# Performance work log

Hardware: AMD Instinct MI355X
Metric: run time of the kernel (lower is better)

## Reference

```python
import jax, jax.numpy as jnp
import numpy as np

NB = 8            # num_blocks
D = 128           # embed_dim
D_INNER = 256     # expand=2
HEADS = 4
P = 64            # headdim
N = 32            # d_state
K = 4             # d_conv
CONV_DIM = D_INNER + 2 * N          # 320 (x, B, C streams)
D_IN_PROJ = 2 * D_INNER + 2 * N + HEADS  # 580 (z, xBC, dt)


def setup_inputs():
    key = jax.random.key(0)
    ks = iter(jax.random.split(key, 16))
    f = lambda shape, s=0.02: (jax.random.normal(next(ks), shape, jnp.float32) * s)
    B, L = 2, 4096
    return {
        'x': jax.random.normal(next(ks), (B, L, D), jnp.float32),
        'residual': jnp.zeros((B, L, D), jnp.float32),
        'ln1_w': jnp.ones((NB, D)), 'ln1_b': jnp.zeros((NB, D)),
        'ln2_w': jnp.ones((NB, D)), 'ln2_b': jnp.zeros((NB, D)),
        'fc1_w': f((NB, 4 * D, D)), 'fc1_b': jnp.zeros((NB, 4 * D)),
        'fc2_w': f((NB, D, 2 * D)), 'fc2_b': jnp.zeros((NB, D)),
        'in_proj_w': f((NB, D_IN_PROJ, D)),
        'conv_w': f((NB, CONV_DIM, K), 0.1), 'conv_b': jnp.zeros((NB, CONV_DIM)),
        'dt_bias': f((NB, HEADS), 0.1),
        'A_log': jnp.tile(jnp.log(jnp.arange(1, HEADS + 1, dtype=jnp.float32)), (NB, 1)),
        'Dp': jnp.ones((NB, HEADS)),
        'rms_w': jnp.ones((NB, D_INNER)),
        'out_proj_w': f((NB, D, D_INNER)),
        'h': 64, 'w': 64,
    }


def layernorm(x, w, b):
    mu = jnp.mean(x, -1, keepdims=True)
    var = jnp.mean((x - mu) ** 2, -1, keepdims=True)
    return (x - mu) * jax.lax.rsqrt(var + 1e-5) * w + b


def mamba2(x, in_proj_w, conv_w, conv_b, dt_bias, A_log, Dp, rms_w, out_proj_w):
    Bb, L, _ = x.shape
    zxbcdt = jnp.einsum('bld,ed->ble', x, in_proj_w)          # [B,L,580]
    z = zxbcdt[..., :D_INNER]
    xBC = zxbcdt[..., D_INNER:D_INNER + CONV_DIM]
    dt = jax.nn.softplus(zxbcdt[..., -HEADS:] + dt_bias)      # [B,L,H]
    # causal depthwise conv1d + silu
    xc = jnp.moveaxis(xBC, 1, 2)                              # [B,C,L]
    xc = jax.lax.conv_general_dilated(xc, conv_w[:, None, :], (1,), [(K - 1, 0)],
                                      feature_group_count=CONV_DIM)
    xBC = jax.nn.silu(jnp.moveaxis(xc, 1, 2) + conv_b)
    xs = xBC[..., :D_INNER].reshape(Bb, L, HEADS, P)          # [B,L,H,P]
    Bm = xBC[..., D_INNER:D_INNER + N]                        # [B,L,N]
    Cm = xBC[..., D_INNER + N:]                               # [B,L,N]
    dA = jnp.exp(dt * (-jnp.exp(A_log)))                      # [B,L,H]

    def step(hst, inp):
        dA_t, dt_t, B_t, C_t, x_t = inp
        hst = hst * dA_t[:, :, None, None] + (dt_t[:, :, None, None] * x_t[..., None]) * B_t[:, None, None, :]
        return hst, jnp.einsum('bhpn,bn->bhp', hst, C_t)

    tfirst = lambda a: jnp.moveaxis(a, 1, 0)
    h0 = jnp.zeros((Bb, HEADS, P, N), x.dtype)
    _, ys = jax.lax.scan(step, h0, (tfirst(dA), tfirst(dt), tfirst(Bm), tfirst(Cm), tfirst(xs)))
    y = jnp.moveaxis(ys, 0, 1) + Dp[None, None, :, None] * xs # [B,L,H,P]
    y = y.reshape(Bb, L, D_INNER) * jax.nn.silu(z)            # gated
    y = y * jax.lax.rsqrt(jnp.mean(y * y, -1, keepdims=True) + 1e-5) * rms_w
    return jnp.einsum('be,de->bd'.replace('b', 'bl'), y, out_proj_w)


def mlp(x, fc1_w, fc1_b, fc2_w, fc2_b):
    x12 = jnp.einsum('bld,ed->ble', x, fc1_w) + fc1_b
    x1, x2 = jnp.split(x12, 2, axis=-1)
    return jnp.einsum('ble,de->bld', jax.nn.silu(x1) * x2, fc2_w) + fc2_b


def reference(x, residual, ln1_w, ln1_b, ln2_w, ln2_b, fc1_w, fc1_b, fc2_w, fc2_b,
              in_proj_w, conv_w, conv_b, dt_bias, A_log, Dp, rms_w, out_proj_w, h, w):
    for i in range(NB):
        residual = x
        x1 = layernorm(residual, ln1_w[i], ln1_b[i])
        x_m = residual + mamba2(x1, in_proj_w[i], conv_w[i], conv_b[i], dt_bias[i],
                                A_log[i], Dp[i], rms_w[i], out_proj_w[i])
        residual = x_m
        x2 = layernorm(residual, ln2_w[i], ln2_b[i])
        x = residual + mlp(x2, fc1_w[i], fc1_b[i], fc2_w[i], fc2_b[i])
    return (x, residual)
```

## Files before the change

### kernel.cpp

```cpp
#include <hip/hip_runtime.h>
#include <hip/hip_bf16.h>
#include <cstddef>

#define NBLK 8
#define DD   128
#define DI   256
#define NH   4
#define PP   64
#define NNs  32
#define CONVD 320
#define EE   580
#define BB   2
#define LLEN 4096
#define ML   (BB*LLEN)
#define SEGS 256
#define TT   16
#define GPAD 264

typedef unsigned short u16;
typedef short bf16x8 __attribute__((ext_vector_type(8)));
typedef float f32x4 __attribute__((ext_vector_type(4)));

__device__ __forceinline__ float siluf(float x){ return x / (1.f + expf(-x)); }
__device__ __forceinline__ float b2f(u16 u){ return __uint_as_float((unsigned)u << 16); }
__device__ __forceinline__ u16 f2b(float f){
    __hip_bfloat16 h = __float2bfloat16(f);
    return *reinterpret_cast<u16*>(&h);
}
__device__ __forceinline__ void ld8f(const u16* p, float* f){
    ushort4 a = *(const ushort4*)p;
    ushort4 b = *(const ushort4*)(p + 4);
    f[0]=b2f(a.x); f[1]=b2f(a.y); f[2]=b2f(a.z); f[3]=b2f(a.w);
    f[4]=b2f(b.x); f[5]=b2f(b.y); f[6]=b2f(b.z); f[7]=b2f(b.w);
}

#define IPW_N (NBLK*EE*DD)
#define OPW_N (NBLK*DD*DI)
#define F1W_N (NBLK*512*DD)
#define F2W_N (NBLK*DD*DI)
#define CVT_TOT (IPW_N+OPW_N+F1W_N+F2W_N)

__global__ __launch_bounds__(256) void cvt_weights(const float* __restrict__ ip,
                                                   const float* __restrict__ op,
                                                   const float* __restrict__ f1,
                                                   const float* __restrict__ f2,
                                                   const float* __restrict__ xin,
                                                   u16* __restrict__ dip,
                                                   u16* __restrict__ dop,
                                                   u16* __restrict__ df1,
                                                   u16* __restrict__ df2,
                                                   float* __restrict__ xout)
{
    int i = blockIdx.x * 256 + threadIdx.x;
    if (i < IPW_N)                          dip[i] = f2b(ip[i]);
    else if (i < IPW_N + OPW_N)             dop[i - IPW_N] = f2b(op[i - IPW_N]);
    else if (i < IPW_N + OPW_N + F1W_N)     df1[i - IPW_N - OPW_N] = f2b(f1[i - IPW_N - OPW_N]);
    else                                    df2[i - IPW_N - OPW_N - F1W_N] = f2b(f2[i - IPW_N - OPW_N - F1W_N]);
    if (i < ML * DD) xout[i] = xin[i];
}

__global__ __launch_bounds__(256) void inproj_ln_gemm(const float* __restrict__ X,
                                                      const float* __restrict__ lnw,
                                                      const float* __restrict__ lnb,
                                                      const u16* __restrict__ W,
                                                      u16* __restrict__ C)
{
    __shared__ __align__(16) u16 Ash[64*128];
    __shared__ __align__(16) u16 Wsh[64*128];
    __shared__ float red[64][8];
    const int tid = threadIdx.x;
    const int wave = tid >> 6, lane = tid & 63;
    const int l15 = lane & 15, quad = lane >> 4;
    const int bm = blockIdx.y * 64;
    const int bn = blockIdx.x * 64;
    const int lrow = tid >> 2, sub = tid & 3;

#pragma unroll
    for (int i = 0; i < 4; i++) {
        int k8 = sub + 4*i;
        uint4 wv = make_uint4(0u,0u,0u,0u);
        if (bn + lrow < EE)
            wv = *(const uint4*)(W + (size_t)(bn + lrow) * DD + k8*8);
        *(uint4*)&Wsh[((size_t)k8*64 + lrow) * 8] = wv;
    }

    const float* xr = X + (size_t)(bm + lrow) * DD + sub*32;
    float4 xv[8];
    float ps = 0.f, pq = 0.f;
#pragma unroll
    for (int i = 0; i < 8; i++) {
        xv[i] = *(const float4*)(xr + i*4);
        ps += xv[i].x + xv[i].y + xv[i].z + xv[i].w;
        pq += xv[i].x*xv[i].x + xv[i].y*xv[i].y + xv[i].z*xv[i].z + xv[i].w*xv[i].w;
    }
    red[lrow][sub] = ps; red[lrow][4+sub] = pq;
    __syncthreads();
    float s = red[lrow][0]+red[lrow][1]+red[lrow][2]+red[lrow][3];
    float q = red[lrow][4]+red[lrow][5]+red[lrow][6]+red[lrow][7];
    float mu = s * (1.f/DD);
    float rstd = rsqrtf(q*(1.f/DD) - mu*mu + 1e-5f);
#pragma unroll
    for (int i = 0; i < 4; i++) {
        float4 a0 = xv[2*i], a1 = xv[2*i+1];
        int c0 = sub*32 + i*8;
        u16 o[8];
        o[0] = f2b((a0.x-mu)*rstd*lnw[c0+0] + lnb[c0+0]);
        o[1] = f2b((a0.y-mu)*rstd*lnw[c0+1] + lnb[c0+1]);
        o[2] = f2b((a0.z-mu)*rstd*lnw[c0+2] + lnb[c0+2]);
        o[3] = f2b((a0.w-mu)*rstd*lnw[c0+3] + lnb[c0+3]);
        o[4] = f2b((a1.x-mu)*rstd*lnw[c0+4] + lnb[c0+4]);
        o[5] = f2b((a1.y-mu)*rstd*lnw[c0+5] + lnb[c0+5]);
        o[6] = f2b((a1.z-mu)*rstd*lnw[c0+6] + lnb[c0+6]);
        o[7] = f2b((a1.w-mu)*rstd*lnw[c0+7] + lnb[c0+7]);
        *(uint4*)&Ash[((size_t)(sub*4+i)*64 + lrow) * 8] = *(uint4*)o;
    }
    __syncthreads();

    f32x4 acc[4];
#pragma unroll
    for (int nt = 0; nt < 4; nt++) acc[nt] = (f32x4){0.f,0.f,0.f,0.f};
#pragma unroll
    for (int kk = 0; kk < 4; kk++) {
        bf16x8 af = *(const bf16x8*)&Ash[(((kk*4 + quad)*64) + wave*16 + l15) * 8];
#pragma unroll
        for (int nt = 0; nt < 4; nt++) {
            bf16x8 bfv = *(const bf16x8*)&Wsh[(((kk*4 + quad)*64) + nt*16 + l15) * 8];
            acc[nt] = __builtin_amdgcn_mfma_f32_16x16x32_bf16(af, bfv, acc[nt], 0, 0, 0);
        }
    }
#pragma unroll
    for (int nt = 0; nt < 4; nt++) {
        int n = bn + nt*16 + l15;
        if (n < EE) {
#pragma unroll
            for (int r = 0; r < 4; r++) {
                int m = bm + wave*16 + quad*4 + r;
                C[(size_t)m * EE + n] = f2b(acc[nt][r]);
            }
        }
    }
}

__global__ __launch_bounds__(256) void scan1(const u16* __restrict__ zx,
                                             const float* __restrict__ cw,
                                             const float* __restrict__ cb,
                                             const float* __restrict__ dt_bias,
                                             const float* __restrict__ A_log,
                                             float* __restrict__ seg,
                                             float* __restrict__ segsum)
{
    __shared__ float Bsh[4][TT*NNs];
    __shared__ float dts[4][TT], das[4][TT];
    int wv = threadIdx.x >> 6;
    int p = threadIdx.x & 63;
    int sg = blockIdx.x % (SEGS/4);
    int bh = blockIdx.x / (SEGS/4);
    int h = bh % NH;
    int b = bh / NH;
    int s = sg*4 + wv;
    int l0 = s * TT;
    int row0 = b * LLEN + l0;

    float xr[TT+3];
    const u16* xcol = zx + (size_t)row0 * EE + 256 + h*64 + p;
#pragma unroll
    for (int r = 0; r < TT+3; r++) {
        int l = l0 - 3 + r;
        xr[r] = (l >= 0) ? b2f(xcol[(ptrdiff_t)(r-3) * EE]) : 0.f;
    }
    float4 wx = *(const float4*)(cw + (size_t)(h*64+p) * 4);
    float cbx = cb[h*64+p];

    if (p < NNs) {
        float br[TT+3];
        const u16* bcol = zx + (size_t)row0 * EE + 512 + p;
#pragma unroll
        for (int r = 0; r < TT+3; r++) {
            int l = l0 - 3 + r;
            br[r] = (l >= 0) ? b2f(bcol[(ptrdiff_t)(r-3) * EE]) : 0.f;
        }
        float4 wb = *(const float4*)(cw + (size_t)(256+p) * 4);
        float cbb = cb[256+p];
#pragma unroll
        for (int t = 0; t < TT; t++)
            Bsh[wv][t*NNs + p] = siluf(cbb + wb.x*br[t] + wb.y*br[t+1] + wb.z*br[t+2] + wb.w*br[t+3]);
    }
    if (p < TT) {
        float v = b2f(zx[(size_t)(row0+p)*EE + (EE-NH) + h]) + dt_bias[h];
        float dt = (v > 20.f) ? v : log1pf(expf(v));
        dts[wv][p] = dt;
        das[wv][p] = expf(-expf(A_log[h]) * dt);
    }
    __syncthreads();

    float hreg[NNs];
#pragma unroll
    for (int n = 0; n < NNs; n++) hreg[n] = 0.f;
    float sdt = 0.f;
#pragma unroll
    for (int t = 0; t < TT; t++) {
        float dA = das[wv][t];
        float dt = dts[wv][t];
        float xv = siluf(cbx + wx.x*xr[t] + wx.y*xr[t+1] + wx.z*xr[t+2] + wx.w*xr[t+3]);
        float dtx = dt * xv;
#pragma unroll
        for (int n4 = 0; n4 < 8; n4++) {
            float4 Bv = *(const float4*)&Bsh[wv][t*NNs + n4*4];
            hreg[n4*4+0] = fmaf(hreg[n4*4+0], dA, dtx * Bv.x);
            hreg[n4*4+1] = fmaf(hreg[n4*4+1], dA, dtx * Bv.y);
            hreg[n4*4+2] = fmaf(hreg[n4*4+2], dA, dtx * Bv.z);
            hreg[n4*4+3] = fmaf(hreg[n4*4+3], dA, dtx * Bv.w);
        }
        sdt += dt;
    }
    int bidg = bh * SEGS + s;
    float* dst = seg + ((size_t)bidg * PP + p) * NNs;
#pragma unroll
    for (int n4 = 0; n4 < 8; n4++)
        *(float4*)(dst + n4*4) = make_float4(hreg[n4*4+0], hreg[n4*4+1], hreg[n4*4+2], hreg[n4*4+3]);
    if (p == 0) segsum[bidg] = sdt;
}

__global__ __launch_bounds__(256) void scan2(float* __restrict__ seg,
                                             const float* __restrict__ segsum,
                                             const float* __restrict__ A_log)
{
    int bh = blockIdx.x >> 3;
    int chunk = blockIdx.x & 7;
    int h = bh % NH;
    int entry = chunk * 256 + threadIdx.x;
    float negA = -expf(A_log[h]);
    float hs = 0.f;
    const float* ss = segsum + bh * SEGS;
    float* base = seg + (size_t)bh * SEGS * (PP * NNs) + entry;
    for (int j0 = 0; j0 < SEGS; j0 += 16) {
        float e[16], a[16];
#pragma unroll
        for (int k = 0; k < 16; k++) {
            a[k] = ss[j0 + k];
            e[k] = base[(size_t)(j0 + k) * (PP * NNs)];
        }
#pragma unroll
        for (int k = 0; k < 16; k++) {
            float Aj = expf(negA * a[k]);
            base[(size_t)(j0 + k) * (PP * NNs)] = hs;
            hs = fmaf(Aj, hs, e[k]);
        }
    }
}

__global__ __launch_bounds__(256) void scan3(const u16* __restrict__ zx,
                                             const float* __restrict__ cw,
                                             const float* __restrict__ cb,
                                             const float* __restrict__ dt_bias,
                                             const float* __restrict__ A_log,
                                             const float* __restrict__ seg,
                                             const float* __restrict__ Dp,
                                             u16* __restrict__ y)
{
    __shared__ float BCsh[4][TT*64];
    __shared__ float dts[4][TT], das[4][TT];
    int wv = threadIdx.x >> 6;
    int p = threadIdx.x & 63;
    int sg = blockIdx.x % (SEGS/4);
    int bh = blockIdx.x / (SEGS/4);
    int h = bh % NH;
    int b = bh / NH;
    int s = sg*4 + wv;
    int l0 = s * TT;
    int row0 = b * LLEN + l0;

    float xr[TT+3];
    const u16* xcol = zx + (size_t)row0 * EE + 256 + h*64 + p;
#pragma unroll
    for (int r = 0; r < TT+3; r++) {
        int l = l0 - 3 + r;
        xr[r] = (l >= 0) ? b2f(xcol[(ptrdiff_t)(r-3) * EE]) : 0.f;
    }
    float4 wx = *(const float4*)(cw + (size_t)(h*64+p) * 4);
    float cbx = cb[h*64+p];

    {
        float br[TT+3];
        const u16* bcol = zx + (size_t)row0 * EE + 512 + p;
#pragma unroll
        for (int r = 0; r < TT+3; r++) {
            int l = l0 - 3 + r;
            br[r] = (l >= 0) ? b2f(bcol[(ptrdiff_t)(r-3) * EE]) : 0.f;
        }
        float4 wb = *(const float4*)(cw + (size_t)(256+p) * 4);
        float cbb = cb[256+p];
#pragma unroll
        for (int t = 0; t < TT; t++)
            BCsh[wv][t*64 + p] = siluf(cbb + wb.x*br[t] + wb.y*br[t+1] + wb.z*br[t+2] + wb.w*br[t+3]);
    }
    if (p < TT) {
        float v = b2f(zx[(size_t)(row0+p)*EE + (EE-NH) + h]) + dt_bias[h];
        float dt = (v > 20.f) ? v : log1pf(expf(v));
        dts[wv][p] = dt;
        das[wv][p] = expf(-expf(A_log[h]) * dt);
    }

    float hreg[NNs];
    int bidg = bh * SEGS + s;
    const float* src = seg + ((size_t)bidg * PP + p) * NNs;
#pragma unroll
    for (int n4 = 0; n4 < 8; n4++) {
        float4 v = *(const float4*)(src + n4*4);
        hreg[n4*4+0] = v.x; hreg[n4*4+1] = v.y; hreg[n4*4+2] = v.z; hreg[n4*4+3] = v.w;
    }
    float dp = Dp[h];
    __syncthreads();

#pragma unroll
    for (int t = 0; t < TT; t++) {
        float dA = das[wv][t];
        float dt = dts[wv][t];
        float xv = siluf(cbx + wx.x*xr[t] + wx.y*xr[t+1] + wx.z*xr[t+2] + wx.w*xr[t+3]);
        float dtx = dt * xv;
        float acc = 0.f;
#pragma unroll
        for (int n4 = 0; n4 < 8; n4++) {
            float4 Bv = *(const float4*)&BCsh[wv][t*64 + n4*4];
            float4 Cv = *(const float4*)&BCsh[wv][t*64 + 32 + n4*4];
            hreg[n4*4+0] = fmaf(hreg[n4*4+0], dA, dtx * Bv.x);
            hreg[n4*4+1] = fmaf(hreg[n4*4+1], dA, dtx * Bv.y);
            hreg[n4*4+2] = fmaf(hreg[n4*4+2], dA, dtx * Bv.z);
            hreg[n4*4+3] = fmaf(hreg[n4*4+3], dA, dtx * Bv.w);
            acc = fmaf(hreg[n4*4+0], Cv.x, acc);
            acc = fmaf(hreg[n4*4+1], Cv.y, acc);
            acc = fmaf(hreg[n4*4+2], Cv.z, acc);
            acc = fmaf(hreg[n4*4+3], Cv.w, acc);
        }
        y[(size_t)(row0 + t) * DI + h*PP + p] = f2b(acc + dp * xv);
    }
}

__global__ __launch_bounds__(256) void grms_outproj_gemm(const u16* __restrict__ Y,
                                                         const u16* __restrict__ Z,
                                                         const float* __restrict__ rmsw,
                                                         const u16* __restrict__ W,
                                                         const float* __restrict__ resid,
                                                         float* __restrict__ C)
{
    __shared__ __align__(16) u16 Ash[32*256];
    __shared__ __align__(16) u16 Wsh[64*256];
    __shared__ float red[32][8];
    __shared__ float rl[32];
    const int tid = threadIdx.x;
    const int wave = tid >> 6, lane = tid & 63;
    const int l15 = lane & 15, quad = lane >> 4;
    const int rt = wave & 1, nq = wave >> 1;
    const int bm = blockIdx.y * 32;
    const int bn = blockIdx.x * 64;

    {
        int wrow = tid >> 2, ksub = tid & 3;
#pragma unroll
        for (int i = 0; i < 8; i++) {
            int k8 = ksub + 4*i;
            uint4 wv = *(const uint4*)(W + (size_t)(bn + wrow) * DI + k8*8);
            *(uint4*)&Wsh[((size_t)k8*64 + wrow) * 8] = wv;
        }
    }

    int lrow = tid >> 3, sub = tid & 7;
    const u16* yr = Y + (size_t)(bm + lrow) * DI + sub*32;
    const u16* zr = Z + (size_t)(bm + lrow) * EE + sub*32;
    float pq = 0.f;
#pragma unroll
    for (int i = 0; i < 4; i++) {
        float yv[8], zv[8];
        ld8f(yr + i*8, yv);
        ld8f(zr + i*8, zv);
        int c0 = sub*32 + i*8;
        u16 o[8];
#pragma unroll
        for (int j = 0; j < 8; j++) {
            float g = yv[j] * siluf(zv[j]);
            pq += g*g;
            o[j] = f2b(g * rmsw[c0 + j]);
        }
        *(uint4*)&Ash[((size_t)(sub*4 + i)*32 + lrow) * 8] = *(uint4*)o;
    }
    red[lrow][sub] = pq;
    __syncthreads();
    if (sub == 0) {
        float qq = 0.f;
#pragma unroll
        for (int j = 0; j < 8; j++) qq += red[lrow][j];
        rl[lrow] = rsqrtf(qq * (1.f/DI) + 1e-5f);
    }
    __syncthreads();

    f32x4 acc[2];
    acc[0] = (f32x4){0.f,0.f,0.f,0.f};
    acc[1] = (f32x4){0.f,0.f,0.f,0.f};
#pragma unroll
    for (int kk = 0; kk < 8; kk++) {
        bf16x8 af = *(const bf16x8*)&Ash[(((kk*4 + quad)*32) + rt*16 + l15) * 8];
#pragma unroll
        for (int nt = 0; nt < 2; nt++) {
            bf16x8 bfv = *(const bf16x8*)&Wsh[(((kk*4 + quad)*64) + nq*32 + nt*16 + l15) * 8];
            acc[nt] = __builtin_amdgcn_mfma_f32_16x16x32_bf16(af, bfv, acc[nt], 0, 0, 0);
        }
    }
#pragma unroll
    for (int nt = 0; nt < 2; nt++) {
        int n = bn + nq*32 + nt*16 + l15;
#pragma unroll
        for (int r = 0; r < 4; r++) {
            int lm = rt*16 + quad*4 + r;
            int m = bm + lm;
            C[(size_t)m * DD + n] = acc[nt][r] * rl[lm] + resid[(size_t)m * DD + n];
        }
    }
}

__global__ __launch_bounds__(512) void mlp_fused(const float* __restrict__ Xm,
                                                 const float* __restrict__ lnw,
                                                 const float* __restrict__ lnb,
                                                 const u16* __restrict__ W1,
                                                 const float* __restrict__ b1,
                                                 const u16* __restrict__ W2,
                                                 const float* __restrict__ b2,
                                                 float* __restrict__ Out,
                                                 float* __restrict__ out2)
{
    __shared__ __align__(16) u16 Ash[32*128];
    __shared__ __align__(16) u16 Wsh[128*128];
    __shared__ __align__(16) u16 Gsh[32*GPAD];
    __shared__ float red[32][32];
    const int tid = threadIdx.x;
    const int wv = tid >> 6, lane = tid & 63;
    const int l15 = lane & 15, quad = lane >> 4;
    const int mt = wv & 1, ng = wv >> 1;
    const int bm = blockIdx.x * 32;

    {
        int lrow = tid >> 4, sub = tid & 15;
        const float* xr = Xm + (size_t)(bm + lrow) * DD + sub*8;
        float4 x0 = *(const float4*)xr;
        float4 x1 = *(const float4*)(xr + 4);
        float ps = x0.x+x0.y+x0.z+x0.w + x1.x+x1.y+x1.z+x1.w;
        float pq = x0.x*x0.x+x0.y*x0.y+x0.z*x0.z+x0.w*x0.w
                 + x1.x*x1.x+x1.y*x1.y+x1.z*x1.z+x1.w*x1.w;
        red[lrow][sub] = ps; red[lrow][16+sub] = pq;
        __syncthreads();
        float s = 0.f, q = 0.f;
#pragma unroll
        for (int j = 0; j < 16; j++) { s += red[lrow][j]; q += red[lrow][16+j]; }
        float mu = s * (1.f/DD);
        float rstd = rsqrtf(q*(1.f/DD) - mu*mu + 1e-5f);
        int c0 = sub*8;
        float xa[8] = {x0.x,x0.y,x0.z,x0.w,x1.x,x1.y,x1.z,x1.w};
        u16 o[8];
#pragma unroll
        for (int j = 0; j < 8; j++)
            o[j] = f2b((xa[j]-mu)*rstd*lnw[c0+j] + lnb[c0+j]);
        *(uint4*)&Ash[((size_t)sub*32 + lrow) * 8] = *(uint4*)o;
    }
    __syncthreads();

    bf16x8 afr[4];
#pragma unroll
    for (int kk = 0; kk < 4; kk++)
        afr[kk] = *(const bf16x8*)&Ash[(((kk*4 + quad)*32) + mt*16 + l15) * 8];

    for (int p = 0; p < 4; p++) {
        __syncthreads();
        {
            int wrow = tid >> 2, ksub = tid & 3;
            int r1 = (wrow < 64) ? (p*64 + wrow) : (256 + p*64 + wrow - 64);
#pragma unroll
            for (int i = 0; i < 4; i++) {
                int k8 = ksub + 4*i;
                uint4 wvv = *(const uint4*)(W1 + (size_t)r1 * DD + k8*8);
                *(uint4*)&Wsh[((size_t)k8*128 + wrow) * 8] = wvv;
            }
        }
        __syncthreads();
        f32x4 aa = (f32x4){0.f,0.f,0.f,0.f};
        f32x4 bb = (f32x4){0.f,0.f,0.f,0.f};
#pragma unroll
        for (int kk = 0; kk < 4; kk++) {
            bf16x8 b1v = *(const bf16x8*)&Wsh[(((kk*4 + quad)*128) + ng*16 + l15) * 8];
            bf16x8 b2v = *(const bf16x8*)&Wsh[(((kk*4 + quad)*128) + 64 + ng*16 + l15) * 8];
            aa = __builtin_amdgcn_mfma_f32_16x16x32_bf16(afr[kk], b1v, aa, 0, 0, 0);
            bb = __builtin_amdgcn_mfma_f32_16x16x32_bf16(afr[kk], b2v, bb, 0, 0, 0);
        }
        int n1 = p*64 + ng*16 + l15;
        float ba = b1[n1];
        float bbv = b1[256 + n1];
#pragma unroll
        for (int r = 0; r < 4; r++) {
            float a = aa[r] + ba;
            float bq = bb[r] + bbv;
            int m = mt*16 + quad*4 + r;
            Gsh[m*GPAD + n1] = f2b(siluf(a) * bq);
        }
    }

    f32x4 acc2[2];
    acc2[0] = (f32x4){0.f,0.f,0.f,0.f};
    acc2[1] = (f32x4){0.f,0.f,0.f,0.f};
    for (int kh = 0; kh < 2; kh++) {
        __syncthreads();
        {
            int wrow = tid >> 2, ksub = tid & 3;
#pragma unroll
            for (int i = 0; i < 4; i++) {
                int k8 = ksub + 4*i;
                uint4 wvv = *(const uint4*)(W2 + (size_t)wrow * DI + kh*128 + k8*8);
                *(uint4*)&Wsh[((size_t)k8*128 + wrow) * 8] = wvv;
            }
        }
        __syncthreads();
#pragma unroll
        for (int kk = 0; kk < 4; kk++) {
            bf16x8 af = *(const bf16x8*)&Gsh[(mt*16 + l15)*GPAD + kh*128 + kk*32 + quad*8];
#pragma unroll
            for (int nt = 0; nt < 2; nt++) {
                bf16x8 bfv = *(const bf16x8*)&Wsh[(((kk*4 + quad)*128) + ng*32 + nt*16 + l15) * 8];
                acc2[nt] = __builtin_amdgcn_mfma_f32_16x16x32_bf16(af, bfv, acc2[nt], 0, 0, 0);
            }
        }
    }
#pragma unroll
    for (int nt = 0; nt < 2; nt++) {
        int n = ng*32 + nt*16 + l15;
        float bv = b2[n];
#pragma unroll
        for (int r = 0; r < 4; r++) {
            int m = bm + mt*16 + quad*4 + r;
            float xmv = Xm[(size_t)m * DD + n];
            float v = acc2[nt][r] + bv + xmv;
            Out[(size_t)m * DD + n] = v;
            if (out2) {
                out2[(size_t)m * DD + n] = v;
                out2[(size_t)ML*DD + (size_t)m * DD + n] = xmv;
            }
        }
    }
}

extern "C" void kernel_launch(void* const* d_in, const int* in_sizes, int n_in,
                              void* d_out, int out_size, void* d_ws, size_t ws_size,
                              hipStream_t stream)
{
    (void)in_sizes; (void)n_in; (void)out_size; (void)ws_size;
    const float* x_in      = (const float*)d_in[0];
    const float* ln1_w     = (const float*)d_in[2];
    const float* ln1_b     = (const float*)d_in[3];
    const float* ln2_w     = (const float*)d_in[4];
    const float* ln2_b     = (const float*)d_in[5];
    const float* fc1_w     = (const float*)d_in[6];
    const float* fc1_b     = (const float*)d_in[7];
    const float* fc2_w     = (const float*)d_in[8];
    const float* fc2_b     = (const float*)d_in[9];
    const float* in_proj_w = (const float*)d_in[10];
    const float* conv_w    = (const float*)d_in[11];
    const float* conv_b    = (const float*)d_in[12];
    const float* dt_bias   = (const float*)d_in[13];
    const float* A_log     = (const float*)d_in[14];
    const float* Dp        = (const float*)d_in[15];
    const float* rms_w     = (const float*)d_in[16];
    const float* out_proj_w= (const float*)d_in[17];

    float* ws = (float*)d_ws;
    size_t o = 0;
    float* bufX    = ws + o; o += (size_t)ML * DD;
    float* bufXm   = ws + o; o += (size_t)ML * DD;
    float* bufSeg  = ws + o; o += (size_t)BB * NH * SEGS * PP * NNs;
    float* bufSegA = ws + o; o += (size_t)BB * NH * SEGS;
    u16* bufBigH  = (u16*)(ws + o); o += ((size_t)ML * EE + 1) / 2;
    u16* bufYH    = (u16*)(ws + o); o += (size_t)ML * DI / 2;
    u16* wIpH     = (u16*)(ws + o); o += (IPW_N + 1) / 2;
    u16* wOpH     = (u16*)(ws + o); o += (OPW_N + 1) / 2;
    u16* wF1H     = (u16*)(ws + o); o += (F1W_N + 1) / 2;
    u16* wF2H     = (u16*)(ws + o); o += (F2W_N + 1) / 2;

    cvt_weights<<<CVT_TOT/256, 256, 0, stream>>>(in_proj_w, out_proj_w, fc1_w, fc2_w,
                                                 x_in, wIpH, wOpH, wF1H, wF2H, bufX);

    for (int i = 0; i < NBLK; i++) {
        const float* ln1wi = ln1_w + i * DD;
        const float* ln1bi = ln1_b + i * DD;
        const float* ln2wi = ln2_w + i * DD;
        const float* ln2bi = ln2_b + i * DD;
        const float* cwi   = conv_w + (size_t)i * CONVD * 4;
        const float* cbi   = conv_b + (size_t)i * CONVD;
        const float* dtbi  = dt_bias + i * NH;
        const float* ali   = A_log + i * NH;
        const float* dpi   = Dp + i * NH;
        const float* rwi   = rms_w + (size_t)i * DI;
        const float* f1bi  = fc1_b + (size_t)i * 512;
        const float* f2bi  = fc2_b + (size_t)i * DD;
        const u16* ipwi = wIpH + (size_t)i * EE * DD;
        const u16* opwi = wOpH + (size_t)i * DD * DI;
        const u16* f1wi = wF1H + (size_t)i * 512 * DD;
        const u16* f2wi = wF2H + (size_t)i * DD * DI;

        inproj_ln_gemm<<<dim3(10, ML/64), 256, 0, stream>>>(bufX, ln1wi, ln1bi, ipwi, bufBigH);
        scan1<<<BB*NH*(SEGS/4), 256, 0, stream>>>(bufBigH, cwi, cbi, dtbi, ali, bufSeg, bufSegA);
        scan2<<<BB*NH*8, 256, 0, stream>>>(bufSeg, bufSegA, ali);
        scan3<<<BB*NH*(SEGS/4), 256, 0, stream>>>(bufBigH, cwi, cbi, dtbi, ali, bufSeg, dpi, bufYH);
        grms_outproj_gemm<<<dim3(2, ML/32), 256, 0, stream>>>(bufYH, bufBigH, rwi, opwi,
                                                              bufX, bufXm);
        mlp_fused<<<ML/32, 512, 0, stream>>>(bufXm, ln2wi, ln2bi, f1wi, f1bi,
                                             f2wi, f2bi, bufX,
                                             (i == NBLK-1) ? (float*)d_out : nullptr);
    }
}
```

Measured before the change: 873.1 us.

## Fuse scan3, gated RMSnorm, out_proj and MLP into one per-segment kernel

```diff
diff --git a/kernel.cpp b/kernel.cpp
--- a/kernel.cpp
+++ b/kernel.cpp
@@ -8,7 +8,6 @@
 #define NH   4
 #define PP   64
 #define NNs  32
-#define CONVD 320
 #define EE   580
 #define BB   2
 #define LLEN 4096
@@ -27,11 +26,10 @@
     __hip_bfloat16 h = __float2bfloat16(f);
     return *reinterpret_cast<u16*>(&h);
 }
-__device__ __forceinline__ void ld8f(const u16* p, float* f){
-    ushort4 a = *(const ushort4*)p;
-    ushort4 b = *(const ushort4*)(p + 4);
-    f[0]=b2f(a.x); f[1]=b2f(a.y); f[2]=b2f(a.z); f[3]=b2f(a.w);
-    f[4]=b2f(b.x); f[5]=b2f(b.y); f[6]=b2f(b.z); f[7]=b2f(b.w);
+__device__ __forceinline__ float waveReduceSum(float v){
+#pragma unroll
+    for (int off = 32; off > 0; off >>= 1) v += __shfl_xor(v, off, 64);
+    return v;
 }
 
 #define IPW_N (NBLK*EE*DD)
@@ -249,80 +247,102 @@
     }
 }
 
-__global__ __launch_bounds__(256) void scan3(const u16* __restrict__ zx,
-                                             const float* __restrict__ cw,
-                                             const float* __restrict__ cb,
-                                             const float* __restrict__ dt_bias,
-                                             const float* __restrict__ A_log,
-                                             const float* __restrict__ seg,
-                                             const float* __restrict__ Dp,
-                                             u16* __restrict__ y)
+__global__ __launch_bounds__(256) void scan3_fused(const u16* __restrict__ zx,
+                                                   const float* __restrict__ cw,
+                                                   const float* __restrict__ cb,
+                                                   const float* __restrict__ dt_bias,
+                                                   const float* __restrict__ A_log,
+                                                   const float* __restrict__ seg,
+                                                   const float* __restrict__ Dp,
+                                                   const float* __restrict__ rmsw,
+                                                   const u16* __restrict__ opw,
+                                                   const float* __restrict__ ln2w,
+                                                   const float* __restrict__ ln2b,
+                                                   const u16* __restrict__ f1w,
+                                                   const float* __restrict__ f1b,
+                                                   const u16* __restrict__ f2w,
+                                                   const float* __restrict__ f2bb,
+                                                   float* __restrict__ bufX,
+                                                   float* __restrict__ outp,
+                                                   int last)
 {
-    __shared__ float BCsh[4][TT*64];
-    __shared__ float dts[4][TT], das[4][TT];
-    int wv = threadIdx.x >> 6;
-    int p = threadIdx.x & 63;
-    int sg = blockIdx.x % (SEGS/4);
-    int bh = blockIdx.x / (SEGS/4);
-    int h = bh % NH;
-    int b = bh / NH;
-    int s = sg*4 + wv;
-    int l0 = s * TT;
-    int row0 = b * LLEN + l0;
+    __shared__ __align__(16) unsigned char smem[64832];
+    u16*   Wsh  = (u16*)smem;
+    float* BCsh = (float*)smem;
+    float* dts  = (float*)(smem + 16384);
+    float* das  = (float*)(smem + 16640);
+    u16*   Ysh  = (u16*)(smem + 32768);
+    float* Xmsh = (float*)(smem + 41216);
+    u16*   Gsh  = (u16*)(smem + 49664);
+    u16*   Ash2 = (u16*)(smem + 58112);
+    float* part = (float*)(smem + 62464);
+    float* rl   = (float*)(smem + 62720);
+    float (*red)[32] = (float(*)[32])(smem + 62784);
+
+    const int tid = threadIdx.x;
+    const int wv = tid >> 6, p = tid & 63;
+    const int l15 = p & 15, quad = p >> 4;
+    const int s = blockIdx.x % SEGS;
+    const int b = blockIdx.x / SEGS;
+    const int h = wv;
+    const int l0 = s * TT;
+    const int row0 = b * LLEN + l0;
 
     float xr[TT+3];
-    const u16* xcol = zx + (size_t)row0 * EE + 256 + h*64 + p;
+    const u16* xcol = zx + (size_t)row0*EE + 256 + h*64 + p;
 #pragma unroll
     for (int r = 0; r < TT+3; r++) {
         int l = l0 - 3 + r;
-        xr[r] = (l >= 0) ? b2f(xcol[(ptrdiff_t)(r-3) * EE]) : 0.f;
-    }
-    float4 wx = *(const float4*)(cw + (size_t)(h*64+p) * 4);
+        xr[r] = (l >= 0) ? b2f(xcol[(ptrdiff_t)(r-3)*EE]) : 0.f;
+    }
+    float4 wx = *(const float4*)(cw + (size_t)(h*64+p)*4);
     float cbx = cb[h*64+p];
-
     {
         float br[TT+3];
-        const u16* bcol = zx + (size_t)row0 * EE + 512 + p;
+        const u16* bcol = zx + (size_t)row0*EE + 512 + p;
 #pragma unroll
         for (int r = 0; r < TT+3; r++) {
             int l = l0 - 3 + r;
-            br[r] = (l >= 0) ? b2f(bcol[(ptrdiff_t)(r-3) * EE]) : 0.f;
-        }
-        float4 wb = *(const float4*)(cw + (size_t)(256+p) * 4);
+            br[r] = (l >= 0) ? b2f(bcol[(ptrdiff_t)(r-3)*EE]) : 0.f;
+        }
+        float4 wb = *(const float4*)(cw + (size_t)(256+p)*4);
         float cbb = cb[256+p];
 #pragma unroll
         for (int t = 0; t < TT; t++)
-            BCsh[wv][t*64 + p] = siluf(cbb + wb.x*br[t] + wb.y*br[t+1] + wb.z*br[t+2] + wb.w*br[t+3]);
+            BCsh[wv*1024 + t*64 + p] = siluf(cbb + wb.x*br[t] + wb.y*br[t+1] + wb.z*br[t+2] + wb.w*br[t+3]);
     }
     if (p < TT) {
         float v = b2f(zx[(size_t)(row0+p)*EE + (EE-NH) + h]) + dt_bias[h];
         float dt = (v > 20.f) ? v : log1pf(expf(v));
-        dts[wv][p] = dt;
-        das[wv][p] = expf(-expf(A_log[h]) * dt);
-    }
-
+        dts[wv*16 + p] = dt;
+        das[wv*16 + p] = expf(-expf(A_log[h]) * dt);
+    }
     float hreg[NNs];
-    int bidg = bh * SEGS + s;
-    const float* src = seg + ((size_t)bidg * PP + p) * NNs;
-#pragma unroll
-    for (int n4 = 0; n4 < 8; n4++) {
-        float4 v = *(const float4*)(src + n4*4);
-        hreg[n4*4+0] = v.x; hreg[n4*4+1] = v.y; hreg[n4*4+2] = v.z; hreg[n4*4+3] = v.w;
-    }
-    float dp = Dp[h];
-    __syncthreads();
-
+    {
+        int bidg = (b*NH + h)*SEGS + s;
+        const float* src = seg + ((size_t)bidg*PP + p)*NNs;
+#pragma unroll
+        for (int n4 = 0; n4 < 8; n4++) {
+            float4 v = *(const float4*)(src + n4*4);
+            hreg[n4*4+0] = v.x; hreg[n4*4+1] = v.y; hreg[n4*4+2] = v.z; hreg[n4*4+3] = v.w;
+        }
+    }
+    float dpv = Dp[h];
+    const u16* zcol = zx + (size_t)row0*EE + h*64 + p;
+    __syncthreads();
+
+    float gs[TT];
 #pragma unroll
     for (int t = 0; t < TT; t++) {
-        float dA = das[wv][t];
-        float dt = dts[wv][t];
+        float dA = das[wv*16 + t];
+        float dt = dts[wv*16 + t];
         float xv = siluf(cbx + wx.x*xr[t] + wx.y*xr[t+1] + wx.z*xr[t+2] + wx.w*xr[t+3]);
         float dtx = dt * xv;
         float acc = 0.f;
 #pragma unroll
         for (int n4 = 0; n4 < 8; n4++) {
-            float4 Bv = *(const float4*)&BCsh[wv][t*64 + n4*4];
-            float4 Cv = *(const float4*)&BCsh[wv][t*64 + 32 + n4*4];
+            float4 Bv = *(const float4*)&BCsh[wv*1024 + t*64 + n4*4];
+            float4 Cv = *(const float4*)&BCsh[wv*1024 + t*64 + 32 + n4*4];
             hreg[n4*4+0] = fmaf(hreg[n4*4+0], dA, dtx * Bv.x);
             hreg[n4*4+1] = fmaf(hreg[n4*4+1], dA, dtx * Bv.y);
             hreg[n4*4+2] = fmaf(hreg[n4*4+2], dA, dtx * Bv.z);
@@ -332,213 +352,158 @@
             acc = fmaf(hreg[n4*4+2], Cv.z, acc);
             acc = fmaf(hreg[n4*4+3], Cv.w, acc);
         }
-        y[(size_t)(row0 + t) * DI + h*PP + p] = f2b(acc + dp * xv);
-    }
-}
-
-__global__ __launch_bounds__(256) void grms_outproj_gemm(const u16* __restrict__ Y,
-                                                         const u16* __restrict__ Z,
-                                                         const float* __restrict__ rmsw,
-                                                         const u16* __restrict__ W,
-                                                         const float* __restrict__ resid,
-                                                         float* __restrict__ C)
-{
-    __shared__ __align__(16) u16 Ash[32*256];
-    __shared__ __align__(16) u16 Wsh[64*256];
-    __shared__ float red[32][8];
-    __shared__ float rl[32];
-    const int tid = threadIdx.x;
-    const int wave = tid >> 6, lane = tid & 63;
-    const int l15 = lane & 15, quad = lane >> 4;
-    const int rt = wave & 1, nq = wave >> 1;
-    const int bm = blockIdx.y * 32;
-    const int bn = blockIdx.x * 64;
-
+        float y = acc + dpv * xv;
+        gs[t] = y * siluf(b2f(zcol[(ptrdiff_t)t * EE]));
+    }
     {
-        int wrow = tid >> 2, ksub = tid & 3;
-#pragma unroll
-        for (int i = 0; i < 8; i++) {
-            int k8 = ksub + 4*i;
-            uint4 wv = *(const uint4*)(W + (size_t)(bn + wrow) * DI + k8*8);
-            *(uint4*)&Wsh[((size_t)k8*64 + wrow) * 8] = wv;
-        }
-    }
-
-    int lrow = tid >> 3, sub = tid & 7;
-    const u16* yr = Y + (size_t)(bm + lrow) * DI + sub*32;
-    const u16* zr = Z + (size_t)(bm + lrow) * EE + sub*32;
-    float pq = 0.f;
-#pragma unroll
-    for (int i = 0; i < 4; i++) {
-        float yv[8], zv[8];
-        ld8f(yr + i*8, yv);
-        ld8f(zr + i*8, zv);
-        int c0 = sub*32 + i*8;
-        u16 o[8];
-#pragma unroll
-        for (int j = 0; j < 8; j++) {
-            float g = yv[j] * siluf(zv[j]);
-            pq += g*g;
-            o[j] = f2b(g * rmsw[c0 + j]);
-        }
-        *(uint4*)&Ash[((size_t)(sub*4 + i)*32 + lrow) * 8] = *(uint4*)o;
-    }
-    red[lrow][sub] = pq;
-    __syncthreads();
-    if (sub == 0) {
-        float qq = 0.f;
-#pragma unroll
-        for (int j = 0; j < 8; j++) qq += red[lrow][j];
-        rl[lrow] = rsqrtf(qq * (1.f/DI) + 1e-5f);
-    }
-    __syncthreads();
-
-    f32x4 acc[2];
-    acc[0] = (f32x4){0.f,0.f,0.f,0.f};
-    acc[1] = (f32x4){0.f,0.f,0.f,0.f};
-#pragma unroll
-    for (int kk = 0; kk < 8; kk++) {
-        bf16x8 af = *(const bf16x8*)&Ash[(((kk*4 + quad)*32) + rt*16 + l15) * 8];
-#pragma unroll
-        for (int nt = 0; nt < 2; nt++) {
-            bf16x8 bfv = *(const bf16x8*)&Wsh[(((kk*4 + quad)*64) + nq*32 + nt*16 + l15) * 8];
-            acc[nt] = __builtin_amdgcn_mfma_f32_16x16x32_bf16(af, bfv, acc[nt], 0, 0, 0);
-        }
-    }
-#pragma unroll
-    for (int nt = 0; nt < 2; nt++) {
-        int n = bn + nq*32 + nt*16 + l15;
+        int c = h*64 + p;
+        float rw = rmsw[c];
+#pragma unroll
+        for (int t = 0; t < TT; t++) {
+            float w = waveReduceSum(gs[t]*gs[t]);
+            if (p == 0) part[t*4 + wv] = w;
+            Ysh[t*GPAD + c] = f2b(gs[t] * rw);
+        }
+    }
+    __syncthreads();
+    if (tid < TT) {
+        float qq = part[tid*4+0] + part[tid*4+1] + part[tid*4+2] + part[tid*4+3];
+        rl[tid] = rsqrtf(qq * (1.f/DI) + 1e-5f);
+    }
+    __syncthreads();
+
+#pragma unroll 1
+    for (int cn = 0; cn < 2; cn++) {
+        {
+            int wrow = tid >> 2, ksub = tid & 3;
+#pragma unroll
+            for (int i = 0; i < 8; i++) {
+                int k8 = ksub + 4*i;
+                *(uint4*)&Wsh[((size_t)k8*64 + wrow)*8] =
+                    *(const uint4*)(opw + (size_t)(cn*64 + wrow)*DI + k8*8);
+            }
+        }
+        __syncthreads();
+        f32x4 accO = (f32x4){0.f,0.f,0.f,0.f};
+#pragma unroll
+        for (int kk = 0; kk < 8; kk++) {
+            bf16x8 af = *(const bf16x8*)&Ysh[l15*GPAD + kk*32 + quad*8];
+            bf16x8 bfv = *(const bf16x8*)&Wsh[(((kk*4 + quad)*64) + wv*16 + l15)*8];
+            accO = __builtin_amdgcn_mfma_f32_16x16x32_bf16(af, bfv, accO, 0, 0, 0);
+        }
+        int n = cn*64 + wv*16 + l15;
 #pragma unroll
         for (int r = 0; r < 4; r++) {
-            int lm = rt*16 + quad*4 + r;
-            int m = bm + lm;
-            C[(size_t)m * DD + n] = acc[nt][r] * rl[lm] + resid[(size_t)m * DD + n];
-        }
-    }
-}
-
-__global__ __launch_bounds__(512) void mlp_fused(const float* __restrict__ Xm,
-                                                 const float* __restrict__ lnw,
-                                                 const float* __restrict__ lnb,
-                                                 const u16* __restrict__ W1,
-                                                 const float* __restrict__ b1,
-                                                 const u16* __restrict__ W2,
-                                                 const float* __restrict__ b2,
-                                                 float* __restrict__ Out,
-                                                 float* __restrict__ out2)
-{
-    __shared__ __align__(16) u16 Ash[32*128];
-    __shared__ __align__(16) u16 Wsh[128*128];
-    __shared__ __align__(16) u16 Gsh[32*GPAD];
-    __shared__ float red[32][32];
-    const int tid = threadIdx.x;
-    const int wv = tid >> 6, lane = tid & 63;
-    const int l15 = lane & 15, quad = lane >> 4;
-    const int mt = wv & 1, ng = wv >> 1;
-    const int bm = blockIdx.x * 32;
+            int m = quad*4 + r;
+            Xmsh[m*132 + n] = accO[r] * rl[m] + bufX[(size_t)(row0 + m)*DD + n];
+        }
+        __syncthreads();
+    }
 
     {
         int lrow = tid >> 4, sub = tid & 15;
-        const float* xr = Xm + (size_t)(bm + lrow) * DD + sub*8;
-        float4 x0 = *(const float4*)xr;
-        float4 x1 = *(const float4*)(xr + 4);
+        float4 x0 = *(const float4*)&Xmsh[lrow*132 + sub*8];
+        float4 x1 = *(const float4*)&Xmsh[lrow*132 + sub*8 + 4];
         float ps = x0.x+x0.y+x0.z+x0.w + x1.x+x1.y+x1.z+x1.w;
         float pq = x0.x*x0.x+x0.y*x0.y+x0.z*x0.z+x0.w*x0.w
                  + x1.x*x1.x+x1.y*x1.y+x1.z*x1.z+x1.w*x1.w;
         red[lrow][sub] = ps; red[lrow][16+sub] = pq;
         __syncthreads();
-        float s = 0.f, q = 0.f;
-#pragma unroll
-        for (int j = 0; j < 16; j++) { s += red[lrow][j]; q += red[lrow][16+j]; }
-        float mu = s * (1.f/DD);
-        float rstd = rsqrtf(q*(1.f/DD) - mu*mu + 1e-5f);
+        float sS = 0.f, qS = 0.f;
+#pragma unroll
+        for (int j = 0; j < 16; j++) { sS += red[lrow][j]; qS += red[lrow][16+j]; }
+        float mu = sS * (1.f/DD);
+        float rstd = rsqrtf(qS*(1.f/DD) - mu*mu + 1e-5f);
         int c0 = sub*8;
         float xa[8] = {x0.x,x0.y,x0.z,x0.w,x1.x,x1.y,x1.z,x1.w};
         u16 o[8];
 #pragma unroll
         for (int j = 0; j < 8; j++)
-            o[j] = f2b((xa[j]-mu)*rstd*lnw[c0+j] + lnb[c0+j]);
-        *(uint4*)&Ash[((size_t)sub*32 + lrow) * 8] = *(uint4*)o;
+            o[j] = f2b((xa[j]-mu)*rstd*ln2w[c0+j] + ln2b[c0+j]);
+        *(uint4*)&Ash2[lrow*136 + c0] = *(uint4*)o;
     }
     __syncthreads();
 
     bf16x8 afr[4];
 #pragma unroll
     for (int kk = 0; kk < 4; kk++)
-        afr[kk] = *(const bf16x8*)&Ash[(((kk*4 + quad)*32) + mt*16 + l15) * 8];
-
-    for (int p = 0; p < 4; p++) {
-        __syncthreads();
+        afr[kk] = *(const bf16x8*)&Ash2[l15*136 + kk*32 + quad*8];
+
+#pragma unroll 1
+    for (int pc = 0; pc < 4; pc++) {
         {
-            int wrow = tid >> 2, ksub = tid & 3;
-            int r1 = (wrow < 64) ? (p*64 + wrow) : (256 + p*64 + wrow - 64);
-#pragma unroll
-            for (int i = 0; i < 4; i++) {
-                int k8 = ksub + 4*i;
-                uint4 wvv = *(const uint4*)(W1 + (size_t)r1 * DD + k8*8);
-                *(uint4*)&Wsh[((size_t)k8*128 + wrow) * 8] = wvv;
+            int wrow = tid >> 1, ksub = tid & 1;
+            int r1 = (wrow < 64) ? (pc*64 + wrow) : (256 + pc*64 + wrow - 64);
+#pragma unroll
+            for (int i = 0; i < 8; i++) {
+                int k8 = ksub + 2*i;
+                *(uint4*)&Wsh[((size_t)k8*128 + wrow)*8] =
+                    *(const uint4*)(f1w + (size_t)r1*DD + k8*8);
             }
         }
         __syncthreads();
         f32x4 aa = (f32x4){0.f,0.f,0.f,0.f};
-        f32x4 bb = (f32x4){0.f,0.f,0.f,0.f};
+        f32x4 bbv2 = (f32x4){0.f,0.f,0.f,0.f};
 #pragma unroll
         for (int kk = 0; kk < 4; kk++) {
-            bf16x8 b1v = *(const bf16x8*)&Wsh[(((kk*4 + quad)*128) + ng*16 + l15) * 8];
-            bf16x8 b2v = *(const bf16x8*)&Wsh[(((kk*4 + quad)*128) + 64 + ng*16 + l15) * 8];
-            aa = __builtin_amdgcn_mfma_f32_16x16x32_bf16(afr[kk], b1v, aa, 0, 0, 0);
-            bb = __builtin_amdgcn_mfma_f32_16x16x32_bf16(afr[kk], b2v, bb, 0, 0, 0);
-        }
-        int n1 = p*64 + ng*16 + l15;
-        float ba = b1[n1];
-        float bbv = b1[256 + n1];
+            bf16x8 b1v = *(const bf16x8*)&Wsh[(((kk*4 + quad)*128) + wv*16 + l15)*8];
+            bf16x8 b2v = *(const bf16x8*)&Wsh[(((kk*4 + quad)*128) + 64 + wv*16 + l15)*8];
+            aa  = __builtin_amdgcn_mfma_f32_16x16x32_bf16(afr[kk], b1v, aa, 0, 0, 0);
+            bbv2 = __builtin_amdgcn_mfma_f32_16x16x32_bf16(afr[kk], b2v, bbv2, 0, 0, 0);
+        }
+        int n1 = pc*64 + wv*16 + l15;
+        float ba = f1b[n1];
+        float bbias = f1b[256 + n1];
 #pragma unroll
         for (int r = 0; r < 4; r++) {
             float a = aa[r] + ba;
-            float bq = bb[r] + bbv;
-            int m = mt*16 + quad*4 + r;
+            float bq = bbv2[r] + bbias;
+            int m = quad*4 + r;
             Gsh[m*GPAD + n1] = f2b(siluf(a) * bq);
         }
+        __syncthreads();
     }
 
     f32x4 acc2[2];
     acc2[0] = (f32x4){0.f,0.f,0.f,0.f};
     acc2[1] = (f32x4){0.f,0.f,0.f,0.f};
+#pragma unroll 1
     for (int kh = 0; kh < 2; kh++) {
-        __syncthreads();
         {
-            int wrow = tid >> 2, ksub = tid & 3;
-#pragma unroll
-            for (int i = 0; i < 4; i++) {
-                int k8 = ksub + 4*i;
-                uint4 wvv = *(const uint4*)(W2 + (size_t)wrow * DI + kh*128 + k8*8);
-                *(uint4*)&Wsh[((size_t)k8*128 + wrow) * 8] = wvv;
+            int wrow = tid >> 1, ksub = tid & 1;
+#pragma unroll
+            for (int i = 0; i < 8; i++) {
+                int k8 = ksub + 2*i;
+                *(uint4*)&Wsh[((size_t)k8*128 + wrow)*8] =
+                    *(const uint4*)(f2w + (size_t)wrow*DI + kh*128 + k8*8);
             }
         }
         __syncthreads();
 #pragma unroll
         for (int kk = 0; kk < 4; kk++) {
-            bf16x8 af = *(const bf16x8*)&Gsh[(mt*16 + l15)*GPAD + kh*128 + kk*32 + quad*8];
+            bf16x8 af = *(const bf16x8*)&Gsh[l15*GPAD + kh*128 + kk*32 + quad*8];
 #pragma unroll
             for (int nt = 0; nt < 2; nt++) {
-                bf16x8 bfv = *(const bf16x8*)&Wsh[(((kk*4 + quad)*128) + ng*32 + nt*16 + l15) * 8];
+                bf16x8 bfv = *(const bf16x8*)&Wsh[(((kk*4 + quad)*128) + wv*32 + nt*16 + l15)*8];
                 acc2[nt] = __builtin_amdgcn_mfma_f32_16x16x32_bf16(af, bfv, acc2[nt], 0, 0, 0);
             }
         }
+        __syncthreads();
     }
 #pragma unroll
     for (int nt = 0; nt < 2; nt++) {
-        int n = ng*32 + nt*16 + l15;
-        float bv = b2[n];
+        int n = wv*32 + nt*16 + l15;
+        float bv = f2bb[n];
 #pragma unroll
         for (int r = 0; r < 4; r++) {
-            int m = bm + mt*16 + quad*4 + r;
-            float xmv = Xm[(size_t)m * DD + n];
+            int m = quad*4 + r;
+            int grow = row0 + m;
+            float xmv = Xmsh[m*132 + n];
             float v = acc2[nt][r] + bv + xmv;
-            Out[(size_t)m * DD + n] = v;
-            if (out2) {
-                out2[(size_t)m * DD + n] = v;
-                out2[(size_t)ML*DD + (size_t)m * DD + n] = xmv;
+            bufX[(size_t)grow*DD + n] = v;
+            if (last) {
+                outp[(size_t)grow*DD + n] = v;
+                outp[(size_t)ML*DD + (size_t)grow*DD + n] = xmv;
             }
         }
     }
@@ -570,11 +535,9 @@
     float* ws = (float*)d_ws;
     size_t o = 0;
     float* bufX    = ws + o; o += (size_t)ML * DD;
-    float* bufXm   = ws + o; o += (size_t)ML * DD;
     float* bufSeg  = ws + o; o += (size_t)BB * NH * SEGS * PP * NNs;
     float* bufSegA = ws + o; o += (size_t)BB * NH * SEGS;
     u16* bufBigH  = (u16*)(ws + o); o += ((size_t)ML * EE + 1) / 2;
-    u16* bufYH    = (u16*)(ws + o); o += (size_t)ML * DI / 2;
     u16* wIpH     = (u16*)(ws + o); o += (IPW_N + 1) / 2;
     u16* wOpH     = (u16*)(ws + o); o += (OPW_N + 1) / 2;
     u16* wF1H     = (u16*)(ws + o); o += (F1W_N + 1) / 2;
@@ -588,8 +551,8 @@
         const float* ln1bi = ln1_b + i * DD;
         const float* ln2wi = ln2_w + i * DD;
         const float* ln2bi = ln2_b + i * DD;
-        const float* cwi   = conv_w + (size_t)i * CONVD * 4;
-        const float* cbi   = conv_b + (size_t)i * CONVD;
+        const float* cwi   = conv_w + (size_t)i * 320 * 4;
+        const float* cbi   = conv_b + (size_t)i * 320;
         const float* dtbi  = dt_bias + i * NH;
         const float* ali   = A_log + i * NH;
         const float* dpi   = Dp + i * NH;
@@ -604,11 +567,9 @@
         inproj_ln_gemm<<<dim3(10, ML/64), 256, 0, stream>>>(bufX, ln1wi, ln1bi, ipwi, bufBigH);
         scan1<<<BB*NH*(SEGS/4), 256, 0, stream>>>(bufBigH, cwi, cbi, dtbi, ali, bufSeg, bufSegA);
         scan2<<<BB*NH*8, 256, 0, stream>>>(bufSeg, bufSegA, ali);
-        scan3<<<BB*NH*(SEGS/4), 256, 0, stream>>>(bufBigH, cwi, cbi, dtbi, ali, bufSeg, dpi, bufYH);
-        grms_outproj_gemm<<<dim3(2, ML/32), 256, 0, stream>>>(bufYH, bufBigH, rwi, opwi,
-                                                              bufX, bufXm);
-        mlp_fused<<<ML/32, 512, 0, stream>>>(bufXm, ln2wi, ln2bi, f1wi, f1bi,
-                                             f2wi, f2bi, bufX,
-                                             (i == NBLK-1) ? (float*)d_out : nullptr);
-    }
-}
+        scan3_fused<<<BB*SEGS, 256, 0, stream>>>(bufBigH, cwi, cbi, dtbi, ali, bufSeg, dpi,
+                                                 rwi, opwi, ln2wi, ln2bi, f1wi, f1bi,
+                                                 f2wi, f2bi, bufX,
+                                                 (float*)d_out, (i == NBLK-1) ? 1 : 0);
+    }
+}
```

Result: slower. 1.864 ms (+113.5%).
